# Kernel tuning notes

Measured on AMD Instinct MI355X. Metric: run time of the kernel, lower is better.

The kernel has to match this reference:

```python
import jax, jax.numpy as jnp
import numpy as np

N_NODES = 20000
N_EDGES = 320000
N_GRAPHS = 256
F_NODE = 11
F_TDA = 30
D = 128            # hidden_dim
H = 4              # num_heads
L = 3              # num_layers
T = 6              # number of task heads
NEG_SLOPE = 0.2    # PyG GATConv default leaky_relu slope
LN_EPS = 1e-5


def setup_inputs() -> dict:
    key = jax.random.key(0)
    ks = jax.random.split(key, 40)
    g = lambda i, shape, fan: jax.random.normal(ks[i], shape, jnp.float32) * (1.0 / np.sqrt(fan))
    inp = {}
    inp['x'] = jax.random.normal(ks[0], (N_NODES, F_NODE), jnp.float32)
    inp['edge_index'] = jax.random.randint(ks[1], (2, N_EDGES), 0, N_NODES)
    inp['batch'] = jnp.sort(jax.random.randint(ks[2], (N_NODES,), 0, N_GRAPHS))
    inp['tda'] = jax.random.normal(ks[3], (N_GRAPHS, F_TDA), jnp.float32)
    # input projection
    inp['w_in'] = g(4, (F_NODE, D), F_NODE); inp['b_in'] = jnp.zeros((D,), jnp.float32)
    # stacked GAT layer params (L layers)
    inp['w_gat'] = g(5, (L, D, H * D), D)
    inp['a_src'] = g(6, (L, H, D), D)
    inp['a_dst'] = g(7, (L, H, D), D)
    inp['b_gat'] = jnp.zeros((L, D), jnp.float32)
    inp['ln_w'] = jnp.ones((L, D), jnp.float32)
    inp['ln_b'] = jnp.zeros((L, D), jnp.float32)
    # TDA branch
    inp['w_tda1'] = g(8, (F_TDA, 64), F_TDA); inp['b_tda1'] = jnp.zeros((64,), jnp.float32)
    inp['w_tda2'] = g(9, (64, 64), 64);       inp['b_tda2'] = jnp.zeros((64,), jnp.float32)
    # shared trunk (combined dim = 2*D + 64 = 320)
    inp['w_sh1'] = g(10, (2 * D + 64, 256), 2 * D + 64); inp['b_sh1'] = jnp.zeros((256,), jnp.float32)
    inp['w_sh2'] = g(11, (256, 128), 256);               inp['b_sh2'] = jnp.zeros((128,), jnp.float32)
    # stacked task heads
    inp['w_h1'] = g(12, (T, 128, 64), 128); inp['b_h1'] = jnp.zeros((T, 64), jnp.float32)
    inp['w_h2'] = g(13, (T, 64, 1), 64);    inp['b_h2'] = jnp.zeros((T, 1), jnp.float32)
    return inp


def _gat_layer(h, src, dst, w, a_s, a_d, bias):
    # PyG GATConv(concat=False): per-head transform, edge softmax, mean over heads.
    n = h.shape[0]
    hh = (h @ w).reshape(n, H, D)                       # [N,H,D]
    alpha_s = jnp.einsum('nhd,hd->nh', hh, a_s)         # [N,H]
    alpha_d = jnp.einsum('nhd,hd->nh', hh, a_d)
    e = jax.nn.leaky_relu(alpha_s[src] + alpha_d[dst], NEG_SLOPE)  # [E,H]
    emax = jax.ops.segment_max(e, dst, num_segments=n)  # per-dst softmax (stable)
    a = jnp.exp(e - emax[dst])
    denom = jax.ops.segment_sum(a, dst, num_segments=n)
    a = a / denom[dst]
    msg = hh[src] * a[:, :, None]                       # [E,H,D]
    out = jax.ops.segment_sum(msg, dst, num_segments=n) # [N,H,D]
    return out.mean(axis=1) + bias                      # concat=False -> head mean, then bias


def _layernorm(x, w, b):
    mu = x.mean(-1, keepdims=True)
    var = ((x - mu) ** 2).mean(-1, keepdims=True)
    return (x - mu) * jax.lax.rsqrt(var + LN_EPS) * w + b


def reference(x, edge_index, batch, tda, w_in, b_in, w_gat, a_src, a_dst, b_gat,
              ln_w, ln_b, w_tda1, b_tda1, w_tda2, b_tda2, w_sh1, b_sh1, w_sh2, b_sh2,
              w_h1, b_h1, w_h2, b_h2):
    n = x.shape[0]
    loops = jnp.arange(n)
    src = jnp.concatenate([edge_index[0], loops])  # PyG add_self_loops=True
    dst = jnp.concatenate([edge_index[1], loops])

    h = jax.nn.relu(x @ w_in + b_in)
    for l in range(L):
        res = h
        g = _gat_layer(h, src, dst, w_gat[l], a_src[l], a_dst[l], b_gat[l])
        h = jax.nn.relu(_layernorm(g, ln_w[l], ln_b[l])) + res

    counts = jax.ops.segment_sum(jnp.ones((n,), h.dtype), batch, num_segments=N_GRAPHS)
    x_mean = jax.ops.segment_sum(h, batch, num_segments=N_GRAPHS) / jnp.maximum(counts, 1.0)[:, None]
    x_max = jax.ops.segment_max(h, batch, num_segments=N_GRAPHS)
    x_max = jnp.where(counts[:, None] > 0, x_max, 0.0)
    gnn_out = jnp.concatenate([x_mean, x_max], axis=1)          # [G, 2D]

    tda_out = jax.nn.relu(jax.nn.relu(tda @ w_tda1 + b_tda1) @ w_tda2 + b_tda2)  # [G,64]
    combined = jnp.concatenate([gnn_out, tda_out], axis=1)      # [G, 320]
    shared = jax.nn.relu(jax.nn.relu(combined @ w_sh1 + b_sh1) @ w_sh2 + b_sh2)  # [G,128]

    # task heads stacked on leading axis t (order = target_names order)
    h1 = jax.nn.relu(jnp.einsum('gd,tdk->tgk', shared, w_h1) + b_h1[:, None, :])
    out = jnp.einsum('tgk,tko->tgo', h1, w_h2) + b_h2[:, None, :]
    return out[..., 0]  # [T, G]
```

## Files before the change

kernel.cpp:

```cpp
#include <hip/hip_runtime.h>
#include <hip/hip_bf16.h>
#include <cstdint>
#include <cstddef>

#define N_NODES  20000
#define N_EDGES  320000
#define E_TOTAL  (N_EDGES + N_NODES)
#define N_GRAPHS 256
#define F_NODE   11
#define F_TDA    30
#define DIM      128
#define NHEAD    4
#define NLAYER   3
#define NTASK    6
#define NEG_SLOPE 0.2f
#define LN_EPS   1e-5f
#define CSR_CAP  64

typedef short bf16x8 __attribute__((ext_vector_type(8)));
typedef float f32x4  __attribute__((ext_vector_type(4)));
typedef float f32x2  __attribute__((ext_vector_type(2)));

__device__ inline unsigned short f2b(float f) {
    unsigned int u = __builtin_bit_cast(unsigned int, f);
    u += 0x7fffu + ((u >> 16) & 1u);
    return (unsigned short)(u >> 16);
}
__device__ inline float blo(unsigned int u) { return __builtin_bit_cast(float, u << 16); }
__device__ inline float bhi(unsigned int u) { return __builtin_bit_cast(float, u & 0xffff0000u); }
__device__ inline float b2f(unsigned short b) {
    return __builtin_bit_cast(float, ((unsigned int)b) << 16);
}

__global__ __launch_bounds__(256) void qprep_kernel(const float* __restrict__ w_gat,
                                                    const float* __restrict__ a_src,
                                                    const float* __restrict__ a_dst,
                                                    unsigned short* __restrict__ wt2,
                                                    float* __restrict__ q_s,
                                                    float* __restrict__ q_d) {
    int bx = blockIdx.x;
    int tid = threadIdx.x;
    if (bx < 768) {
        int i = bx * 256 + tid;
        if (i >= NLAYER * 128 * 512) return;
        int l = i >> 16;
        int rem = i & 65535;
        int jcol = rem >> 9;
        int p = rem & 511;
        int lanep = p >> 3, j8 = p & 7;
        int hp = j8 >> 1, bb = j8 & 1;
        int d = lanep * 2 + bb;
        wt2[i] = f2b(w_gat[(size_t)l * 65536 + (size_t)d * 512 + hp * 128 + jcol] * 0.25f);
    } else {
        int bx2 = bx - 768;
        int l = bx2 >> 7, k = bx2 & 127;
        int hh_ = tid >> 6, lane = tid & 63;
        int d0 = lane * 2;
        size_t wb = (size_t)l * 65536 + (size_t)k * 512 + hh_ * 128;
        size_t ab = (size_t)l * 512 + hh_ * 128;
        float ps = w_gat[wb + d0] * a_src[ab + d0] + w_gat[wb + d0 + 1] * a_src[ab + d0 + 1];
        float pd = w_gat[wb + d0] * a_dst[ab + d0] + w_gat[wb + d0 + 1] * a_dst[ab + d0 + 1];
#pragma unroll
        for (int off = 32; off; off >>= 1) { ps += __shfl_xor(ps, off); pd += __shfl_xor(pd, off); }
        if (lane == 0) {
            q_s[(size_t)(l * 128 + k) * 4 + hh_] = ps;
            q_d[(size_t)(l * 128 + k) * 4 + hh_] = pd;
        }
    }
}

__global__ __launch_bounds__(256) void prep_kernel(const float* __restrict__ x,
                                                   const float* __restrict__ w,
                                                   const float* __restrict__ b,
                                                   unsigned short* __restrict__ h_bf,
                                                   const float* __restrict__ q_s,
                                                   const float* __restrict__ q_d,
                                                   float4* __restrict__ als4,
                                                   float4* __restrict__ ald4,
                                                   const int* __restrict__ edge_index,
                                                   int* __restrict__ degs,
                                                   int* __restrict__ csr_src) {
    int bx = blockIdx.x;
    int tid = threadIdx.x;
    if (bx < 2500) {
        __shared__ float xr[8][F_NODE];
        __shared__ float vbuf[8][128];
        __shared__ float qs_t[512];
        __shared__ float qd_t[512];
        qs_t[tid] = q_s[tid]; qs_t[256 + tid] = q_s[256 + tid];
        qd_t[tid] = q_d[tid]; qd_t[256 + tid] = q_d[256 + tid];
        if (tid < 8 * F_NODE) {
            int nl = tid / F_NODE, k = tid % F_NODE;
            xr[nl][k] = x[(size_t)(bx * 8 + nl) * F_NODE + k];
        }
        __syncthreads();
        int d = tid & 127;
        int halfsel = tid >> 7;
#pragma unroll
        for (int p = 0; p < 4; p++) {
            int nl = p * 2 + halfsel;
            float acc = b[d];
#pragma unroll
            for (int k = 0; k < F_NODE; k++) acc += xr[nl][k] * w[k * DIM + d];
            float v = fmaxf(acc, 0.f);
            h_bf[(size_t)(bx * 8 + nl) * DIM + d] = f2b(v);
            vbuf[nl][d] = v;
        }
        __syncthreads();
        int wave = tid >> 6, lane = tid & 63;
#pragma unroll
        for (int t = 0; t < 2; t++) {
            int nl = wave * 2 + t;
            int n = bx * 8 + nl;
            float2 v2 = *(const float2*)&vbuf[nl][2 * lane];
            int k4 = 2 * lane * 4;
            float ps[4], pd[4];
#pragma unroll
            for (int hh_ = 0; hh_ < 4; hh_++) {
                ps[hh_] = v2.x * qs_t[k4 + hh_] + v2.y * qs_t[k4 + 4 + hh_];
                pd[hh_] = v2.x * qd_t[k4 + hh_] + v2.y * qd_t[k4 + 4 + hh_];
            }
#pragma unroll
            for (int off = 32; off; off >>= 1) {
#pragma unroll
                for (int hh_ = 0; hh_ < 4; hh_++) {
                    ps[hh_] += __shfl_xor(ps[hh_], off);
                    pd[hh_] += __shfl_xor(pd[hh_], off);
                }
            }
            if (lane == 0) {
                als4[n] = make_float4(ps[0], ps[1], ps[2], ps[3]);
                ald4[n] = make_float4(pd[0], pd[1], pd[2], pd[3]);
            }
        }
    } else {
        int base = (bx - 2500) * 1024;
#pragma unroll
        for (int k = 0; k < 4; k++) {
            int e = base + k * 256 + tid;
            if (e < E_TOTAL) {
                int s, d;
                if (e < N_EDGES) { s = edge_index[e]; d = edge_index[N_EDGES + e]; }
                else             { s = e - N_EDGES;   d = s; }
                int pos = atomicAdd(&degs[d], 1);
                if (pos < CSR_CAP) csr_src[d * CSR_CAP + pos] = s;
            }
        }
    }
}

template<int LYR>
__global__ __launch_bounds__(256) void agg2_kernel(const unsigned short* __restrict__ h_bf,
                                                   const float4* __restrict__ als4,
                                                   const float4* __restrict__ ald4,
                                                   const int* __restrict__ degs,
                                                   const int* __restrict__ csr_src,
                                                   unsigned short* __restrict__ z) {
    int wave = threadIdx.x >> 6, lane = threadIdx.x & 63;
    int n = blockIdx.x * 4 + wave;
    if (n >= N_NODES) return;

    int deg = degs[n];
    const int* __restrict__ srcp = csr_src + (size_t)n * CSR_CAP;
    const unsigned int* __restrict__ h32 = (const unsigned int*)h_bf;
    const float* __restrict__ als_f = (const float*)als4;
    float4 ad = ald4[n];

    int l4 = lane & 3;
    int le = (lane >> 2) & 3;
    float adh = (l4 == 0) ? ad.x : ((l4 == 1) ? ad.y : ((l4 == 2) ? ad.z : ad.w));

    f32x2 acc2[4] = {};
    float lsOwn = 0.f;

    int s0 = 0, s1 = 0, s2 = 0, s3 = 0;
    if (deg >= 4) { s0 = srcp[0]; s1 = srcp[1]; s2 = srcp[2]; s3 = srcp[3]; }
    int e = 0;
    for (; e + 4 <= deg; ) {
        int c0 = s0, c1 = s1, c2 = s2, c3 = s3;
        unsigned int hv0 = h32[(size_t)c0 * 64 + lane];
        unsigned int hv1 = h32[(size_t)c1 * 64 + lane];
        unsigned int hv2 = h32[(size_t)c2 * 64 + lane];
        unsigned int hv3 = h32[(size_t)c3 * 64 + lane];
        int se = (le == 0) ? c0 : ((le == 1) ? c1 : ((le == 2) ? c2 : c3));
        float a = als_f[(size_t)se * 4 + l4];
        int en = e + 4;
        if (en + 4 <= deg) { s0 = srcp[en]; s1 = srcp[en + 1]; s2 = srcp[en + 2]; s3 = srcp[en + 3]; }
        float v = a + adh;
        v = fmaxf(v, NEG_SLOPE * v);
        float w = __expf(fminf(v, 60.f));
        lsOwn += w;
        float wv[16];
#pragma unroll
        for (int j = 0; j < 16; j++) wv[j] = __shfl(w, j);
        unsigned int hv[4] = { hv0, hv1, hv2, hv3 };
#pragma unroll
        for (int j = 0; j < 4; j++) {
            f32x2 f; f.x = blo(hv[j]); f.y = bhi(hv[j]);
            acc2[0] += wv[j * 4 + 0] * f;
            acc2[1] += wv[j * 4 + 1] * f;
            acc2[2] += wv[j * 4 + 2] * f;
            acc2[3] += wv[j * 4 + 3] * f;
        }
        e = en;
    }
    float ls[4];
#pragma unroll
    for (int hh_ = 0; hh_ < 4; hh_++) {
        ls[hh_] = __shfl(lsOwn, hh_) + __shfl(lsOwn, 4 + hh_)
                + __shfl(lsOwn, 8 + hh_) + __shfl(lsOwn, 12 + hh_);
    }
    for (; e < deg; e++) {
        int s = srcp[e];
        float4 a4 = als4[s];
        unsigned int vv = h32[(size_t)s * 64 + lane];
        f32x2 f; f.x = blo(vv); f.y = bhi(vv);
#pragma unroll
        for (int hh_ = 0; hh_ < 4; hh_++) {
            float v = (&a4.x)[hh_] + (&ad.x)[hh_];
            v = (v > 0.f) ? v : NEG_SLOPE * v;
            float w = __expf(fminf(v, 60.f));
            ls[hh_] += w;
            acc2[hh_] += w * f;
        }
    }
    uint4 pb;
    unsigned int* pc = &pb.x;
#pragma unroll
    for (int hh_ = 0; hh_ < 4; hh_++) {
        float il = 1.f / ls[hh_];
        pc[hh_] = (unsigned)f2b(acc2[hh_].x * il) | ((unsigned)f2b(acc2[hh_].y * il) << 16);
    }
    *(uint4*)(z + (size_t)n * 512 + lane * 8) = pb;
}

template<int LYR>
__global__ __launch_bounds__(256) void zgemm_kernel(const unsigned short* __restrict__ z,
                                                    const unsigned short* __restrict__ wt2_l,
                                                    const float* __restrict__ b_gat,
                                                    const float* __restrict__ ln_w,
                                                    const float* __restrict__ ln_b,
                                                    const unsigned short* __restrict__ hb_in,
                                                    unsigned short* __restrict__ hb_out,
                                                    const float* __restrict__ q_s_next,
                                                    const float* __restrict__ q_d_next,
                                                    float4* __restrict__ als4,
                                                    float4* __restrict__ ald4,
                                                    int M) {
    __shared__ __align__(16) unsigned short As[64 * 136];
    __shared__ __align__(16) unsigned short Bs[128 * 136];
    int tid = threadIdx.x;
    int m0 = blockIdx.x << 6;
    int wave = tid >> 6, lane = tid & 63;
    int lr = lane & 15, lg = lane >> 4;

    const uint4 zero4 = make_uint4(0, 0, 0, 0);
    f32x4 acc[8] = {};
    for (int kc = 0; kc < 4; kc++) {
#pragma unroll
        for (int p = 0; p < 4; p++) {
            int i = p * 256 + tid;
            int row = i >> 4, kg = i & 15;
            int arow = m0 + row;
            uint4 av = (arow < M) ? *(const uint4*)(z + (size_t)arow * 512 + kc * 128 + kg * 8) : zero4;
            *(uint4*)&As[row * 136 + kg * 8] = av;
        }
#pragma unroll
        for (int p = 0; p < 8; p++) {
            int i = p * 256 + tid;
            int row = i >> 4, kg = i & 15;
            uint4 bv = *(const uint4*)(wt2_l + (size_t)row * 512 + kc * 128 + kg * 8);
            *(uint4*)&Bs[row * 136 + kg * 8] = bv;
        }
        __syncthreads();
#pragma unroll
        for (int ks = 0; ks < 4; ks++) {
            bf16x8 af = *(const bf16x8*)&As[(wave * 16 + lr) * 136 + ks * 32 + lg * 8];
#pragma unroll
            for (int nt = 0; nt < 8; nt++) {
                bf16x8 bf_ = *(const bf16x8*)&Bs[(nt * 16 + lr) * 136 + ks * 32 + lg * 8];
                acc[nt] = __builtin_amdgcn_mfma_f32_16x16x32_bf16(af, bf_, acc[nt], 0, 0, 0);
            }
        }
        __syncthreads();
    }

    float bg[8], lnw[8], lnb[8];
#pragma unroll
    for (int nt = 0; nt < 8; nt++) {
        int col = nt * 16 + lr;
        bg[nt] = b_gat[col]; lnw[nt] = ln_w[col]; lnb[nt] = ln_b[col];
    }
    const bool do_alpha = (LYR + 1 < NLAYER);
    float4 qs4[8], qd4[8];
    if (do_alpha) {
#pragma unroll
        for (int nt = 0; nt < 8; nt++) {
            int col = nt * 16 + lr;
            qs4[nt] = *(const float4*)(q_s_next + (size_t)col * 4);
            qd4[nt] = *(const float4*)(q_d_next + (size_t)col * 4);
        }
    }
#pragma unroll
    for (int r = 0; r < 4; r++) {
        int row = m0 + wave * 16 + lg * 4 + r;
        bool valid = (row < M);
        float g[8];
        float s = 0.f;
#pragma unroll
        for (int nt = 0; nt < 8; nt++) { g[nt] = acc[nt][r] + bg[nt]; s += g[nt]; }
#pragma unroll
        for (int off = 1; off < 16; off <<= 1) s += __shfl_xor(s, off);
        float mu = s * (1.f / 128.f);
        float s2 = 0.f;
#pragma unroll
        for (int nt = 0; nt < 8; nt++) { float d = g[nt] - mu; s2 += d * d; }
#pragma unroll
        for (int off = 1; off < 16; off <<= 1) s2 += __shfl_xor(s2, off);
        float rstd = rsqrtf(s2 * (1.f / 128.f) + LN_EPS);
        float o[8];
#pragma unroll
        for (int nt = 0; nt < 8; nt++) {
            int col = nt * 16 + lr;
            float hv = valid ? b2f(hb_in[(size_t)row * 128 + col]) : 0.f;
            o[nt] = fmaxf((g[nt] - mu) * rstd * lnw[nt] + lnb[nt], 0.f) + hv;
            if (valid) hb_out[(size_t)row * 128 + col] = f2b(o[nt]);
        }
        if (do_alpha) {
            float ps[4] = {}, pd[4] = {};
#pragma unroll
            for (int nt = 0; nt < 8; nt++) {
                ps[0] += o[nt] * qs4[nt].x; pd[0] += o[nt] * qd4[nt].x;
                ps[1] += o[nt] * qs4[nt].y; pd[1] += o[nt] * qd4[nt].y;
                ps[2] += o[nt] * qs4[nt].z; pd[2] += o[nt] * qd4[nt].z;
                ps[3] += o[nt] * qs4[nt].w; pd[3] += o[nt] * qd4[nt].w;
            }
#pragma unroll
            for (int off = 1; off < 16; off <<= 1) {
#pragma unroll
                for (int hh_ = 0; hh_ < 4; hh_++) {
                    ps[hh_] += __shfl_xor(ps[hh_], off);
                    pd[hh_] += __shfl_xor(pd[hh_], off);
                }
            }
            if (lr == 0 && valid) {
                als4[row] = make_float4(ps[0], ps[1], ps[2], ps[3]);
                ald4[row] = make_float4(pd[0], pd[1], pd[2], pd[3]);
            }
        }
    }
}

__device__ int lower_bound_dev(const int* a, int n, int v) {
    int lo = 0, hi = n;
    while (lo < hi) { int mid = (lo + hi) >> 1; if (a[mid] < v) lo = mid + 1; else hi = mid; }
    return lo;
}

__global__ __launch_bounds__(512) void pooltail_kernel(
    const unsigned short* __restrict__ h, const int* __restrict__ batch,
    const float* __restrict__ tda,
    const float* __restrict__ w_t1, const float* __restrict__ b_t1,
    const float* __restrict__ w_t2, const float* __restrict__ b_t2,
    const float* __restrict__ w_sh1, const float* __restrict__ b_sh1,
    const float* __restrict__ w_sh2, const float* __restrict__ b_sh2,
    const float* __restrict__ w_h1, const float* __restrict__ b_h1,
    const float* __restrict__ w_h2, const float* __restrict__ b_h2,
    float* __restrict__ out) {
    __shared__ float ssum[4][128];
    __shared__ float smax[4][128];
    __shared__ int bounds[2];
    __shared__ float comb[320];
    __shared__ float tr[F_TDA];
    __shared__ float t1[64];
    __shared__ float s1o[256];
    __shared__ float s2o[128];
    __shared__ float prods[NTASK * 64];
    int g = blockIdx.x, tid = threadIdx.x;

    if (tid < 2) bounds[tid] = lower_bound_dev(batch, N_NODES, g + tid);
    if (tid >= 2 && tid - 2 < F_TDA) tr[tid - 2] = tda[g * F_TDA + (tid - 2)];
    __syncthreads();
    int lo = bounds[0], hi = bounds[1];
    int q = tid >> 7, d = tid & 127;
    float s = 0.f, m = -1e30f;
    for (int i = lo + q; i < hi; i += 4) {
        float v = b2f(h[(size_t)i * DIM + d]);
        s += v; m = fmaxf(m, v);
    }
    ssum[q][d] = s; smax[q][d] = m;
    __syncthreads();
    if (tid < 128) {
        float S = ssum[0][d] + ssum[1][d] + ssum[2][d] + ssum[3][d];
        float M = fmaxf(fmaxf(smax[0][d], smax[1][d]), fmaxf(smax[2][d], smax[3][d]));
        int cnt = hi - lo;
        comb[d] = S / fmaxf((float)cnt, 1.f);
        comb[128 + d] = (cnt > 0) ? M : 0.f;
    } else if (tid >= 128 && tid < 192) {
        int j = tid - 128;
        float a = b_t1[j];
#pragma unroll
        for (int k = 0; k < F_TDA; k++) a += tr[k] * w_t1[k * 64 + j];
        t1[j] = fmaxf(a, 0.f);
    }
    __syncthreads();
    if (tid < 64) {
        float a = b_t2[tid];
#pragma unroll
        for (int k = 0; k < 64; k++) a += t1[k] * w_t2[k * 64 + tid];
        comb[256 + tid] = fmaxf(a, 0.f);
    }
    __syncthreads();
    if (tid < 256) {
        float a = b_sh1[tid];
        for (int k = 0; k < 320; k++) a += comb[k] * w_sh1[k * 256 + tid];
        s1o[tid] = fmaxf(a, 0.f);
    }
    __syncthreads();
    if (tid < 128) {
        float a = b_sh2[tid];
        for (int k = 0; k < 256; k++) a += s1o[k] * w_sh2[k * 128 + tid];
        s2o[tid] = fmaxf(a, 0.f);
    }
    __syncthreads();
    if (tid < NTASK * 64) {
        int t = tid >> 6, k = tid & 63;
        float a = b_h1[t * 64 + k];
#pragma unroll 16
        for (int dd = 0; dd < 128; dd++) a += s2o[dd] * w_h1[(size_t)t * 8192 + dd * 64 + k];
        prods[tid] = fmaxf(a, 0.f) * w_h2[t * 64 + k];
    }
    __syncthreads();
    if (tid < NTASK) {
        float p = b_h2[tid];
#pragma unroll 16
        for (int k = 0; k < 64; k++) p += prods[tid * 64 + k];
        out[tid * 256 + g] = p;
    }
}

extern "C" void kernel_launch(void* const* d_in, const int* in_sizes, int n_in,
                              void* d_out, int out_size, void* d_ws, size_t ws_size,
                              hipStream_t stream) {
    const float* x        = (const float*)d_in[0];
    const int*   edge_idx = (const int*)  d_in[1];
    const int*   batch    = (const int*)  d_in[2];
    const float* tda      = (const float*)d_in[3];
    const float* w_in     = (const float*)d_in[4];
    const float* b_in     = (const float*)d_in[5];
    const float* w_gat    = (const float*)d_in[6];
    const float* a_src    = (const float*)d_in[7];
    const float* a_dst    = (const float*)d_in[8];
    const float* b_gat    = (const float*)d_in[9];
    const float* ln_w     = (const float*)d_in[10];
    const float* ln_b     = (const float*)d_in[11];
    const float* w_tda1   = (const float*)d_in[12];
    const float* b_tda1   = (const float*)d_in[13];
    const float* w_tda2   = (const float*)d_in[14];
    const float* b_tda2   = (const float*)d_in[15];
    const float* w_sh1    = (const float*)d_in[16];
    const float* b_sh1    = (const float*)d_in[17];
    const float* w_sh2    = (const float*)d_in[18];
    const float* b_sh2    = (const float*)d_in[19];
    const float* w_h1     = (const float*)d_in[20];
    const float* b_h1     = (const float*)d_in[21];
    const float* w_h2     = (const float*)d_in[22];
    const float* b_h2     = (const float*)d_in[23];
    float* out = (float*)d_out;

    size_t off = 0;
    auto alloc = [&](size_t bytes) -> void* {
        void* p = (char*)d_ws + off;
        off += (bytes + 255) & ~(size_t)255;
        return p;
    };
    unsigned short* hb_a   = (unsigned short*)alloc((size_t)N_NODES * DIM * 2);
    unsigned short* hb_b   = (unsigned short*)alloc((size_t)N_NODES * DIM * 2);
    unsigned short* z      = (unsigned short*)alloc((size_t)N_NODES * 512 * 2);
    unsigned short* wt2    = (unsigned short*)alloc((size_t)NLAYER * 128 * 512 * 2);
    float*          q_s    = (float*)alloc((size_t)NLAYER * 128 * 4 * 4);
    float*          q_d    = (float*)alloc((size_t)NLAYER * 128 * 4 * 4);
    float4*         als4   = (float4*)alloc((size_t)N_NODES * 16);
    float4*         ald4   = (float4*)alloc((size_t)N_NODES * 16);
    int*            degs   = (int*)  alloc((size_t)N_NODES * 4);
    int*            csrsrc = (int*)  alloc((size_t)N_NODES * CSR_CAP * 4);

    hipMemsetAsync(degs, 0, (size_t)N_NODES * 4, stream);

    qprep_kernel<<<1152, 256, 0, stream>>>(w_gat, a_src, a_dst, wt2, q_s, q_d);

    int sb = (E_TOTAL + 1023) / 1024;
    prep_kernel<<<2500 + sb, 256, 0, stream>>>(x, w_in, b_in, hb_a, q_s, q_d,
                                               als4, ald4, edge_idx, degs, csrsrc);

    int ab = (N_NODES + 3) / 4;
    int gb = (N_NODES + 63) / 64;
    agg2_kernel<0><<<ab, 256, 0, stream>>>(hb_a, als4, ald4, degs, csrsrc, z);
    zgemm_kernel<0><<<gb, 256, 0, stream>>>(z, wt2,
        b_gat, ln_w, ln_b, hb_a, hb_b, q_s + 512, q_d + 512, als4, ald4, N_NODES);
    agg2_kernel<1><<<ab, 256, 0, stream>>>(hb_b, als4, ald4, degs, csrsrc, z);
    zgemm_kernel<1><<<gb, 256, 0, stream>>>(z, wt2 + 65536,
        b_gat + DIM, ln_w + DIM, ln_b + DIM, hb_b, hb_a, q_s + 1024, q_d + 1024,
        als4, ald4, N_NODES);
    agg2_kernel<2><<<ab, 256, 0, stream>>>(hb_a, als4, ald4, degs, csrsrc, z);
    zgemm_kernel<2><<<gb, 256, 0, stream>>>(z, wt2 + 131072,
        b_gat + 2 * DIM, ln_w + 2 * DIM, ln_b + 2 * DIM, hb_a, hb_b,
        nullptr, nullptr, als4, ald4, N_NODES);

    pooltail_kernel<<<N_GRAPHS, 512, 0, stream>>>(
        hb_b, batch, tda, w_tda1, b_tda1, w_tda2, b_tda2,
        w_sh1, b_sh1, w_sh2, b_sh2, w_h1, b_h1, w_h2, b_h2, out);
}
```

Before: 297.9 us.

## Process two nodes per wavefront in GAT aggregation with 8-byte gathers

The aggregation kernel now assigns each half-wavefront (32 lanes) to one destination node, so every lane gathers 4 bf16 features as a uint2 instead of 2. Edge weights are broadcast within each half using ds_bpermute, and a unified masked loop replaces the separate 4-edge main loop and scalar tail. The output channel layout changes to 4 contiguous dims per head per lane, and the weight prepack is reordered to match. The degree memset is folded into the qprep kernel to drop one API call. Both halves now loop to the larger of the two degrees, which wastes some work, and the extra accumulators raise register pressure.

After: 354.1 us. +18.9%, slower.

```diff
diff --git a/kernel.cpp b/kernel.cpp
--- a/kernel.cpp
+++ b/kernel.cpp
@@ -31,13 +31,18 @@
 __device__ inline float b2f(unsigned short b) {
     return __builtin_bit_cast(float, ((unsigned int)b) << 16);
 }
+__device__ inline float bperm_f(int addr, float v) {
+    return __builtin_bit_cast(float,
+        __builtin_amdgcn_ds_bpermute(addr, __builtin_bit_cast(int, v)));
+}
 
 __global__ __launch_bounds__(256) void qprep_kernel(const float* __restrict__ w_gat,
                                                     const float* __restrict__ a_src,
                                                     const float* __restrict__ a_dst,
                                                     unsigned short* __restrict__ wt2,
                                                     float* __restrict__ q_s,
-                                                    float* __restrict__ q_d) {
+                                                    float* __restrict__ q_d,
+                                                    int* __restrict__ degs) {
     int bx = blockIdx.x;
     int tid = threadIdx.x;
     if (bx < 768) {
@@ -47,11 +52,12 @@
         int rem = i & 65535;
         int jcol = rem >> 9;
         int p = rem & 511;
-        int lanep = p >> 3, j8 = p & 7;
-        int hp = j8 >> 1, bb = j8 & 1;
-        int d = lanep * 2 + bb;
+        int lanep = p >> 4;
+        int hp = (p >> 2) & 3;
+        int m = p & 3;
+        int d = lanep * 4 + m;
         wt2[i] = f2b(w_gat[(size_t)l * 65536 + (size_t)d * 512 + hp * 128 + jcol] * 0.25f);
-    } else {
+    } else if (bx < 1152) {
         int bx2 = bx - 768;
         int l = bx2 >> 7, k = bx2 & 127;
         int hh_ = tid >> 6, lane = tid & 63;
@@ -65,6 +71,13 @@
         if (lane == 0) {
             q_s[(size_t)(l * 128 + k) * 4 + hh_] = ps;
             q_d[(size_t)(l * 128 + k) * 4 + hh_] = pd;
+        }
+    } else {
+        int i0 = (bx - 1152) * 1024 + tid;
+#pragma unroll
+        for (int r = 0; r < 4; r++) {
+            int i = i0 + r * 256;
+            if (i < N_NODES) degs[i] = 0;
         }
     }
 }
@@ -157,81 +170,79 @@
                                                    const int* __restrict__ csr_src,
                                                    unsigned short* __restrict__ z) {
     int wave = threadIdx.x >> 6, lane = threadIdx.x & 63;
-    int n = blockIdx.x * 4 + wave;
-    if (n >= N_NODES) return;
+    int half = lane >> 5;
+    int hl = lane & 31;
+    int n = blockIdx.x * 8 + wave * 2 + half;
 
     int deg = degs[n];
+    int degO = __shfl_xor(deg, 32);
+    int mdeg = max(deg, degO);
+
     const int* __restrict__ srcp = csr_src + (size_t)n * CSR_CAP;
     const unsigned int* __restrict__ h32 = (const unsigned int*)h_bf;
     const float* __restrict__ als_f = (const float*)als4;
     float4 ad = ald4[n];
 
-    int l4 = lane & 3;
-    int le = (lane >> 2) & 3;
-    float adh = (l4 == 0) ? ad.x : ((l4 == 1) ? ad.y : ((l4 == 2) ? ad.z : ad.w));
-
-    f32x2 acc2[4] = {};
+    int l4 = hl & 3;
+    int le = (hl >> 2) & 3;
+    float adh = (&ad.x)[l4];
+    int bperm_base = (lane & 32) << 2;
+
+    f32x2 acc2[8] = {};
     float lsOwn = 0.f;
 
-    int s0 = 0, s1 = 0, s2 = 0, s3 = 0;
-    if (deg >= 4) { s0 = srcp[0]; s1 = srcp[1]; s2 = srcp[2]; s3 = srcp[3]; }
-    int e = 0;
-    for (; e + 4 <= deg; ) {
-        int c0 = s0, c1 = s1, c2 = s2, c3 = s3;
-        unsigned int hv0 = h32[(size_t)c0 * 64 + lane];
-        unsigned int hv1 = h32[(size_t)c1 * 64 + lane];
-        unsigned int hv2 = h32[(size_t)c2 * 64 + lane];
-        unsigned int hv3 = h32[(size_t)c3 * 64 + lane];
-        int se = (le == 0) ? c0 : ((le == 1) ? c1 : ((le == 2) ? c2 : c3));
+    for (int e = 0; e < mdeg; e += 4) {
+        int sj[4];
+#pragma unroll
+        for (int j = 0; j < 4; j++) {
+            int idx = e + j;
+            sj[j] = (idx < deg) ? srcp[idx] : 0;
+        }
+        uint2 hv[4];
+#pragma unroll
+        for (int j = 0; j < 4; j++)
+            hv[j] = *(const uint2*)(h32 + (size_t)sj[j] * 64 + hl * 2);
+        int se = sj[le];
         float a = als_f[(size_t)se * 4 + l4];
-        int en = e + 4;
-        if (en + 4 <= deg) { s0 = srcp[en]; s1 = srcp[en + 1]; s2 = srcp[en + 2]; s3 = srcp[en + 3]; }
         float v = a + adh;
         v = fmaxf(v, NEG_SLOPE * v);
         float w = __expf(fminf(v, 60.f));
+        w = (e + le < deg) ? w : 0.f;
         lsOwn += w;
-        float wv[16];
-#pragma unroll
-        for (int j = 0; j < 16; j++) wv[j] = __shfl(w, j);
-        unsigned int hv[4] = { hv0, hv1, hv2, hv3 };
+        float wq[16];
+#pragma unroll
+        for (int q = 0; q < 16; q++)
+            wq[q] = bperm_f(bperm_base + q * 4, w);
 #pragma unroll
         for (int j = 0; j < 4; j++) {
-            f32x2 f; f.x = blo(hv[j]); f.y = bhi(hv[j]);
-            acc2[0] += wv[j * 4 + 0] * f;
-            acc2[1] += wv[j * 4 + 1] * f;
-            acc2[2] += wv[j * 4 + 2] * f;
-            acc2[3] += wv[j * 4 + 3] * f;
-        }
-        e = en;
+            f32x2 f0; f0.x = blo(hv[j].x); f0.y = bhi(hv[j].x);
+            f32x2 f1; f1.x = blo(hv[j].y); f1.y = bhi(hv[j].y);
+#pragma unroll
+            for (int h = 0; h < 4; h++) {
+                float ww = wq[j * 4 + h];
+                acc2[h * 2]     += ww * f0;
+                acc2[h * 2 + 1] += ww * f1;
+            }
+        }
     }
     float ls[4];
 #pragma unroll
-    for (int hh_ = 0; hh_ < 4; hh_++) {
-        ls[hh_] = __shfl(lsOwn, hh_) + __shfl(lsOwn, 4 + hh_)
-                + __shfl(lsOwn, 8 + hh_) + __shfl(lsOwn, 12 + hh_);
-    }
-    for (; e < deg; e++) {
-        int s = srcp[e];
-        float4 a4 = als4[s];
-        unsigned int vv = h32[(size_t)s * 64 + lane];
-        f32x2 f; f.x = blo(vv); f.y = bhi(vv);
-#pragma unroll
-        for (int hh_ = 0; hh_ < 4; hh_++) {
-            float v = (&a4.x)[hh_] + (&ad.x)[hh_];
-            v = (v > 0.f) ? v : NEG_SLOPE * v;
-            float w = __expf(fminf(v, 60.f));
-            ls[hh_] += w;
-            acc2[hh_] += w * f;
-        }
-    }
-    uint4 pb;
-    unsigned int* pc = &pb.x;
-#pragma unroll
-    for (int hh_ = 0; hh_ < 4; hh_++) {
-        float il = 1.f / ls[hh_];
-        pc[hh_] = (unsigned)f2b(acc2[hh_].x * il) | ((unsigned)f2b(acc2[hh_].y * il) << 16);
-    }
-    *(uint4*)(z + (size_t)n * 512 + lane * 8) = pb;
+    for (int h = 0; h < 4; h++) {
+        ls[h] = bperm_f(bperm_base + (h) * 4, lsOwn)
+              + bperm_f(bperm_base + (4 + h) * 4, lsOwn)
+              + bperm_f(bperm_base + (8 + h) * 4, lsOwn)
+              + bperm_f(bperm_base + (12 + h) * 4, lsOwn);
+    }
+    unsigned int pw[8];
+#pragma unroll
+    for (int h = 0; h < 4; h++) {
+        float il = 1.f / ls[h];
+        pw[h * 2]     = (unsigned)f2b(acc2[h * 2].x * il)     | ((unsigned)f2b(acc2[h * 2].y * il) << 16);
+        pw[h * 2 + 1] = (unsigned)f2b(acc2[h * 2 + 1].x * il) | ((unsigned)f2b(acc2[h * 2 + 1].y * il) << 16);
+    }
+    unsigned short* zp = z + (size_t)n * 512 + hl * 16;
+    *(uint4*)zp       = make_uint4(pw[0], pw[1], pw[2], pw[3]);
+    *(uint4*)(zp + 8) = make_uint4(pw[4], pw[5], pw[6], pw[7]);
 }
 
 template<int LYR>
@@ -485,15 +496,13 @@
     int*            degs   = (int*)  alloc((size_t)N_NODES * 4);
     int*            csrsrc = (int*)  alloc((size_t)N_NODES * CSR_CAP * 4);
 
-    hipMemsetAsync(degs, 0, (size_t)N_NODES * 4, stream);
-
-    qprep_kernel<<<1152, 256, 0, stream>>>(w_gat, a_src, a_dst, wt2, q_s, q_d);
+    qprep_kernel<<<1172, 256, 0, stream>>>(w_gat, a_src, a_dst, wt2, q_s, q_d, degs);
 
     int sb = (E_TOTAL + 1023) / 1024;
     prep_kernel<<<2500 + sb, 256, 0, stream>>>(x, w_in, b_in, hb_a, q_s, q_d,
                                                als4, ald4, edge_idx, degs, csrsrc);
 
-    int ab = (N_NODES + 3) / 4;
+    int ab = 2500;
     int gb = (N_NODES + 63) / 64;
     agg2_kernel<0><<<ab, 256, 0, stream>>>(hb_a, als4, ald4, degs, csrsrc, z);
     zgemm_kernel<0><<<gb, 256, 0, stream>>>(z, wt2,
```
